# Optimization experiments

Hardware: AMD Instinct MI355X
Metric: run time of the kernel (lower is better)

## Reference

```python
import jax, jax.numpy as jnp
import numpy as np
from jax import lax

WS = 11
SIGMA = 1.5
C1 = 0.01 ** 2
C2 = 0.03 ** 2


def _gauss_kernel(size=WS, sigma=SIGMA):
    c = jnp.arange(size, dtype=jnp.float32) - size // 2
    g = jnp.exp(-c ** 2 / (2 * sigma ** 2))
    g = g / g.sum()
    k = g[None, :] * g[:, None]              # (ws, ws)
    return k[None, None, :, :]               # (O=1, I=1, ws, ws)


def _depthwise_conv(x, k, C):
    pad = WS // 2
    kC = jnp.broadcast_to(k, (C, 1, WS, WS))  # groups=C depthwise
    return lax.conv_general_dilated(
        x, kC, window_strides=(1, 1), padding=[(pad, pad), (pad, pad)],
        dimension_numbers=('NCHW', 'OIHW', 'NCHW'), feature_group_count=C)


def _ssim_pair(pred, target, k):
    pred = (pred + 1.0) / 2.0
    target = (target + 1.0) / 2.0
    C = pred.shape[1]
    mu1 = _depthwise_conv(pred, k, C)
    mu2 = _depthwise_conv(target, k, C)
    mu1_sq = mu1 * mu1
    mu2_sq = mu2 * mu2
    mu12 = mu1 * mu2
    s1 = _depthwise_conv(pred * pred, k, C) - mu1_sq
    s2 = _depthwise_conv(target * target, k, C) - mu2_sq
    s12 = _depthwise_conv(pred * target, k, C) - mu12
    num = (2.0 * mu12 + C1) * (2.0 * s12 + C2)
    den = (mu1_sq + mu2_sq + C1) * (s1 + s2 + C2)
    return jnp.mean(num / den)


def setup_inputs() -> dict:
    key = jax.random.key(0)
    k1, k2, k3 = jax.random.split(key, 3)
    shape = (16, 1, 512, 512)
    # images in [-1, 1]
    fused = jax.random.uniform(k1, shape, jnp.float32, -1.0, 1.0)
    img_a = jax.random.uniform(k2, shape, jnp.float32, -1.0, 1.0)
    img_b = jax.random.uniform(k3, shape, jnp.float32, -1.0, 1.0)
    return {"fused": fused, "img_a": img_a, "img_b": img_b}


def reference(fused, img_a, img_b):
    k = _gauss_kernel()
    ssim_a = _ssim_pair(fused, img_a, k)
    ssim_b = _ssim_pair(fused, img_b, k)
    return 1.0 - (ssim_a + ssim_b) / 2.0
```

## Files before the change

kernel.cpp:

```cpp
#include <hip/hip_runtime.h>

#define NT 512
#define TW 32
#define TH 32
#define IH (TH + 10)
#define HP 32
#define IMW 512
#define IMH 512
#define NBLK ((IMW / TW) * (IMH / TH) * 16)

typedef float f32x2 __attribute__((ext_vector_type(2)));

__device__ __forceinline__ float wave_reduce(float v) {
    #pragma unroll
    for (int off = 32; off > 0; off >>= 1)
        v += __shfl_down(v, off, 64);
    return v;
}

__device__ __forceinline__ int swz(int i) { return i ^ (i >> 3); }

#define G0 0.00102838f
#define G1 0.00759840f
#define G2 0.03600077f
#define G3 0.10936070f
#define G4 0.21300590f
#define G5 0.26601190f

template<bool BORDER>
__device__ __forceinline__ void h_pass(
    const float* __restrict__ Fp, const float* __restrict__ Ap,
    const float* __restrict__ Bp, int x0, int y0, int tid,
    float4* __restrict__ h4a, float4* __restrict__ h4b)
{
    const float g[11] = {G0, G1, G2, G3, G4, G5, G4, G3, G2, G1, G0};
    if (tid >= IH * 8) return;
    const int r  = tid >> 3;
    const int cg = tid & 7;
    const int gy = y0 + r - 5;
    bool yok = true;
    if (BORDER) yok = (gy >= 0) && (gy < IMH);

    f32x2 accs[4][4];
    #pragma unroll
    for (int k = 0; k < 4; ++k)
        #pragma unroll
        for (int q = 0; q < 4; ++q) accs[k][q] = (f32x2){0.f, 0.f};

    const int xbase = x0 + 4 * cg - 8;
    #pragma unroll
    for (int w = 0; w < 5; ++w) {
        const int xc = xbase + 4 * w;
        float4 p4 = {-1.f, -1.f, -1.f, -1.f};
        float4 a4 = {-1.f, -1.f, -1.f, -1.f};
        float4 b4 = {-1.f, -1.f, -1.f, -1.f};
        bool ld = true;
        if (BORDER) ld = yok && (xc >= 0) && (xc < IMW);
        if (ld) {
            const size_t o = ((size_t)gy * IMW + xc) >> 2;
            p4 = ((const float4*)Fp)[o];
            a4 = ((const float4*)Ap)[o];
            b4 = ((const float4*)Bp)[o];
        }
        const float pe[4] = {p4.x, p4.y, p4.z, p4.w};
        const float ae[4] = {a4.x, a4.y, a4.z, a4.w};
        const float be[4] = {b4.x, b4.y, b4.z, b4.w};
        #pragma unroll
        for (int e = 0; e < 4; ++e) {
            const int i = 4 * w + e;
            if (i < 3 || i >= 17) continue;
            const int t = i - 3;
            const float p = pe[e];
            const float a = ae[e];
            const float b = be[e];
            const f32x2 v_pa   = {p, a};
            const f32x2 v_ab   = {a, b};
            const f32x2 v_pp2  = {p, p};
            const f32x2 v_ppaa = v_pa * v_pa;
            const f32x2 v_papb = v_pp2 * v_ab;
            const f32x2 v_bbb  = {b, b * b};
            #pragma unroll
            for (int k = 0; k < 4; ++k) {
                const int j = t - k;
                if (j < 0 || j > 10) continue;
                const f32x2 w2 = {g[j], g[j]};
                accs[k][0] += w2 * v_pa;
                accs[k][1] += w2 * v_bbb;
                accs[k][2] += w2 * v_ppaa;
                accs[k][3] += w2 * v_papb;
            }
        }
    }
    #pragma unroll
    for (int k = 0; k < 4; ++k) {
        const int sc = swz(4 * cg + k);
        h4a[r * HP + sc] = make_float4(accs[k][0].x, accs[k][0].y,
                                       accs[k][1].x, accs[k][1].y);
        h4b[r * HP + sc] = make_float4(accs[k][2].x, accs[k][2].y,
                                       accs[k][3].x, accs[k][3].y);
    }
}

__global__ __launch_bounds__(NT, 6) void ssim_main_kernel(
    const float* __restrict__ fused,
    const float* __restrict__ img_a,
    const float* __restrict__ img_b,
    float* __restrict__ slots)
{
    __shared__ float4 h4a[IH * HP];
    __shared__ float4 h4b[IH * HP];
    __shared__ float red[NT / 64];

    const float g[11] = {G0, G1, G2, G3, G4, G5, G4, G3, G2, G1, G0};

    const int tid = threadIdx.x;
    const int x0 = blockIdx.x * TW;
    const int y0 = blockIdx.y * TH;
    const size_t ioff = (size_t)blockIdx.z * IMW * IMH;
    const float* Fp = fused + ioff;
    const float* Ap = img_a + ioff;
    const float* Bp = img_b + ioff;

    const bool border = (blockIdx.x == 0) | (blockIdx.x == gridDim.x - 1) |
                        (blockIdx.y == 0) | (blockIdx.y == gridDim.y - 1);
    if (border) h_pass<true >(Fp, Ap, Bp, x0, y0, tid, h4a, h4b);
    else        h_pass<false>(Fp, Ap, Bp, x0, y0, tid, h4a, h4b);
    __syncthreads();

    const float C1v = 1e-4f;
    const float C2v = 9e-4f;
    float lsum = 0.f;
    {
        const int c  = tid & 31;
        const int rg = tid >> 5;
        const int R0 = rg * 2;
        const int sc = swz(c);

        f32x2 m2[2][4];
        #pragma unroll
        for (int k = 0; k < 2; ++k)
            #pragma unroll
            for (int q = 0; q < 4; ++q) m2[k][q] = (f32x2){0.f, 0.f};

        #pragma unroll
        for (int j = 0; j < 12; ++j) {
            const float4 va = h4a[(R0 + j) * HP + sc];
            const float4 vb = h4b[(R0 + j) * HP + sc];
            const f32x2 va01 = {va.x, va.y};
            const f32x2 va23 = {va.z, va.w};
            const f32x2 vb01 = {vb.x, vb.y};
            const f32x2 vb23 = {vb.z, vb.w};
            #pragma unroll
            for (int k = 0; k < 2; ++k) {
                const int t = j - k;
                if (t < 0 || t > 10) continue;
                const f32x2 w2 = {g[t], g[t]};
                m2[k][0] += w2 * va01;
                m2[k][1] += w2 * va23;
                m2[k][2] += w2 * vb01;
                m2[k][3] += w2 * vb23;
            }
        }
        #pragma unroll
        for (int k = 0; k < 2; ++k) {
            const float Mf  = m2[k][0].x, Ma  = m2[k][0].y;
            const float Mb  = m2[k][1].x, Mbb = m2[k][1].y;
            const float Mff = m2[k][2].x, Maa = m2[k][2].y;
            const float Mfa = m2[k][3].x, Mfb = m2[k][3].y;
            const float Fo = Mf + 1.f;
            const float Ao = Ma + 1.f;
            const float Bo = Mb + 1.f;
            const float sp  = fmaf(-Mf, Mf, Mff) * 0.25f;
            const float sa  = fmaf(-Ma, Ma, Maa) * 0.25f;
            const float sb  = fmaf(-Mb, Mb, Mbb) * 0.25f;
            const float spa = fmaf(-Mf, Ma, Mfa) * 0.25f;
            const float spb = fmaf(-Mf, Mb, Mfb) * 0.25f;
            const float Fo2 = Fo * Fo;
            const float na = fmaf(0.5f * Fo, Ao, C1v) * fmaf(2.f, spa, C2v);
            const float da = fmaf(0.25f, fmaf(Ao, Ao, Fo2), C1v) * (sp + sa + C2v);
            const float nb = fmaf(0.5f * Fo, Bo, C1v) * fmaf(2.f, spb, C2v);
            const float db = fmaf(0.25f, fmaf(Bo, Bo, Fo2), C1v) * (sp + sb + C2v);
            lsum += na * __builtin_amdgcn_rcpf(da)
                  + nb * __builtin_amdgcn_rcpf(db);
        }
    }

    lsum = wave_reduce(lsum);
    if ((tid & 63) == 0) red[tid >> 6] = lsum;
    __syncthreads();
    if (tid == 0) {
        float s = 0.f;
        #pragma unroll
        for (int i = 0; i < NT / 64; ++i) s += red[i];
        const int lin = blockIdx.x + (int)gridDim.x * (blockIdx.y + (int)gridDim.y * blockIdx.z);
        slots[lin] = s;
    }
}

__global__ __launch_bounds__(256) void ssim_finalize_kernel(
    const float* __restrict__ slots, float* __restrict__ out, float invTwoN)
{
    __shared__ float red[256 / 64];
    float s = 0.f;
    const float4* s4 = (const float4*)slots;
    for (int i = threadIdx.x; i < NBLK / 4; i += 256) {
        const float4 v = s4[i];
        s += (v.x + v.y) + (v.z + v.w);
    }
    s = wave_reduce(s);
    if ((threadIdx.x & 63) == 0) red[threadIdx.x >> 6] = s;
    __syncthreads();
    if (threadIdx.x == 0)
        out[0] = 1.f - (red[0] + red[1] + red[2] + red[3]) * invTwoN;
}

extern "C" void kernel_launch(void* const* d_in, const int* in_sizes, int n_in,
                              void* d_out, int out_size, void* d_ws, size_t ws_size,
                              hipStream_t stream) {
    const float* fused = (const float*)d_in[0];
    const float* img_a = (const float*)d_in[1];
    const float* img_b = (const float*)d_in[2];
    float* out = (float*)d_out;
    float* slots = (float*)d_ws;

    dim3 grid(IMW / TW, IMH / TH, 16);
    ssim_main_kernel<<<grid, NT, 0, stream>>>(fused, img_a, img_b, slots);

    const float invTwoN = 1.f / (2.f * 16.f * (float)IMW * (float)IMH);
    ssim_finalize_kernel<<<1, 256, 0, stream>>>(slots, out, invTwoN);
}
```

Measured before the change: 111.1 us.

## Stage interior tile inputs in LDS before the horizontal pass

For interior blocks, all threads cooperatively load the 42x48 input halo of all three images into a new LDS buffer with one float4 per thread per image, then the horizontal pass reads from LDS instead of issuing five overlapping global loads per thread. The goal is to cut redundant global/L2 traffic, since neighbouring thread groups previously reread overlapping columns. It adds an extra barrier and 24 KB of shared memory, and lowers the launch-bounds occupancy hint from 6 to 2 blocks per CU, which may reduce latency hiding. Border blocks keep the direct global-load path.

```diff
diff --git a/kernel.cpp b/kernel.cpp
--- a/kernel.cpp
+++ b/kernel.cpp
@@ -30,7 +30,8 @@
 template<bool BORDER>
 __device__ __forceinline__ void h_pass(
     const float* __restrict__ Fp, const float* __restrict__ Ap,
-    const float* __restrict__ Bp, int x0, int y0, int tid,
+    const float* __restrict__ Bp, const float4* __restrict__ raw4,
+    int x0, int y0, int tid,
     float4* __restrict__ h4a, float4* __restrict__ h4b)
 {
     const float g[11] = {G0, G1, G2, G3, G4, G5, G4, G3, G2, G1, G0};
@@ -48,19 +49,25 @@
         for (int q = 0; q < 4; ++q) accs[k][q] = (f32x2){0.f, 0.f};
 
     const int xbase = x0 + 4 * cg - 8;
+    const size_t rowo = (size_t)gy * (IMW / 4) + (xbase >> 2);
+    const int lbase = r * 12 + cg;
+
     #pragma unroll
     for (int w = 0; w < 5; ++w) {
-        const int xc = xbase + 4 * w;
-        float4 p4 = {-1.f, -1.f, -1.f, -1.f};
-        float4 a4 = {-1.f, -1.f, -1.f, -1.f};
-        float4 b4 = {-1.f, -1.f, -1.f, -1.f};
-        bool ld = true;
-        if (BORDER) ld = yok && (xc >= 0) && (xc < IMW);
-        if (ld) {
-            const size_t o = ((size_t)gy * IMW + xc) >> 2;
-            p4 = ((const float4*)Fp)[o];
-            a4 = ((const float4*)Ap)[o];
-            b4 = ((const float4*)Bp)[o];
+        float4 p4, a4, b4;
+        if (BORDER) {
+            p4 = make_float4(-1.f, -1.f, -1.f, -1.f);
+            a4 = p4; b4 = p4;
+            const int xc = xbase + 4 * w;
+            if (yok && (xc >= 0) && (xc < IMW)) {
+                p4 = ((const float4*)Fp)[rowo + w];
+                a4 = ((const float4*)Ap)[rowo + w];
+                b4 = ((const float4*)Bp)[rowo + w];
+            }
+        } else {
+            p4 = raw4[lbase + w];
+            a4 = raw4[512 + lbase + w];
+            b4 = raw4[1024 + lbase + w];
         }
         const float pe[4] = {p4.x, p4.y, p4.z, p4.w};
         const float ae[4] = {a4.x, a4.y, a4.z, a4.w};
@@ -101,12 +108,13 @@
     }
 }
 
-__global__ __launch_bounds__(NT, 6) void ssim_main_kernel(
+__global__ __launch_bounds__(NT, 2) void ssim_main_kernel(
     const float* __restrict__ fused,
     const float* __restrict__ img_a,
     const float* __restrict__ img_b,
     float* __restrict__ slots)
 {
+    __shared__ float4 raw4[1536];
     __shared__ float4 h4a[IH * HP];
     __shared__ float4 h4b[IH * HP];
     __shared__ float red[NT / 64];
@@ -123,8 +131,23 @@
 
     const bool border = (blockIdx.x == 0) | (blockIdx.x == gridDim.x - 1) |
                         (blockIdx.y == 0) | (blockIdx.y == gridDim.y - 1);
-    if (border) h_pass<true >(Fp, Ap, Bp, x0, y0, tid, h4a, h4b);
-    else        h_pass<false>(Fp, Ap, Bp, x0, y0, tid, h4a, h4b);
+
+    if (!border) {
+        const int q  = tid < 504 ? tid : 503;
+        const int qr = q / 12;
+        const int qc = q - qr * 12;
+        const size_t off = (size_t)(y0 - 5 + qr) * (IMW / 4) + (x0 / 4 - 2 + qc);
+        const float4 vF = ((const float4*)Fp)[off];
+        const float4 vA = ((const float4*)Ap)[off];
+        const float4 vB = ((const float4*)Bp)[off];
+        raw4[tid]        = vF;
+        raw4[512 + tid]  = vA;
+        raw4[1024 + tid] = vB;
+    }
+    __syncthreads();
+
+    if (border) h_pass<true >(Fp, Ap, Bp, raw4, x0, y0, tid, h4a, h4b);
+    else        h_pass<false>(Fp, Ap, Bp, raw4, x0, y0, tid, h4a, h4b);
     __syncthreads();
 
     const float C1v = 1e-4f;
```

Result: slower. 118.9 us (+7.0%).
